# Kernel optimization log

Measured on AMD Instinct MI355X. Metric: run time of the kernel, lower is better.

## Reference

```python
import jax, jax.numpy as jnp
import numpy as np
import math

Q_SHAPES = [(20, 30), (10, 15), (5, 8)]
S_SHAPES = [(20, 30), (10, 15), (5, 8)]
C_IN = 256
C_OUT = 256
NUM_HEADS = 8


def _rel_indices(q_shapes, s_shapes):
    # Faithful translation of QSGA.get_rel_indices: block matrix over pyramid levels.
    rows = []
    for hq, wq in q_shapes:
        cols = []
        for hs, ws in s_shapes:
            ind = np.arange(ws)[None, :] / ws - np.arange(hq)[:, None] / hq  # [hq, ws]
            sc = math.sqrt(ws * hq)
            indx = np.tile(ind, (wq, hs)) * sc                              # [hq*wq, hs*ws]
            indy = np.repeat(np.repeat(ind, wq, axis=0), hs, axis=1) * sc   # [hq*wq, hs*ws]
            indd = indx ** 2 + indy ** 2
            cols.append(np.stack([indd, indx, indy], axis=-1))
        rows.append(np.concatenate(cols, axis=1))
    return jnp.asarray(np.concatenate(rows, axis=0)[None].astype(np.float32))  # [1, Nq, Ns, 3]


def setup_inputs() -> dict:
    key = jax.random.key(0)
    ks = jax.random.split(key, 8)
    B, M = 2, 5
    Nq = sum(h * w for h, w in Q_SHAPES)
    Ns = sum(h * w for h, w in S_SHAPES)
    std = 0.02
    # local_init: v = identity, pos_proj weight zero except col0 = -alphas, gating = ones
    min_a, max_a = 0.002, 0.2
    alphas = np.array([min_a + (max_a - min_a) / NUM_HEADS ** 2.5 * i ** 2.5 for i in range(NUM_HEADS)], np.float32)
    Wp = np.zeros((NUM_HEADS, 3), np.float32)
    Wp[:, 0] = -alphas
    return {
        "q_feat": jax.random.normal(ks[0], (B, Nq, C_IN), jnp.float32),
        "s_feat": jax.random.normal(ks[1], (M, Ns, C_IN), jnp.float32),
        "rel_indices": _rel_indices(Q_SHAPES, S_SHAPES),
        "Wq": jax.random.normal(ks[2], (C_OUT, C_IN), jnp.float32) * std,
        "bq": jnp.zeros((C_OUT,), jnp.float32),
        "Wk": jax.random.normal(ks[3], (C_OUT, C_IN), jnp.float32) * std,
        "bk": jnp.zeros((C_OUT,), jnp.float32),
        "Wv": jnp.eye(C_OUT, C_IN, dtype=jnp.float32),
        "bv": jnp.zeros((C_OUT,), jnp.float32),
        "Wp": jnp.asarray(Wp),
        "bp": jnp.zeros((NUM_HEADS,), jnp.float32),
        "Wo": jax.random.normal(ks[4], (C_OUT, C_OUT), jnp.float32) * std,
        "bo": jnp.zeros((C_OUT,), jnp.float32),
        "gating": jnp.ones((NUM_HEADS,), jnp.float32),
    }


def reference(q_feat, s_feat, rel_indices, Wq, bq, Wk, bk, Wv, bv, Wp, bp, Wo, bo, gating):
    B, Nq, _ = q_feat.shape
    M, Ns, _ = s_feat.shape
    H = gating.shape[0]
    C = Wq.shape[0]
    Dh = C // H
    scale = Dh ** -0.5
    # projections -> [B,H,Nq,Dh], [M,H,Ns,Dh]
    q = (q_feat @ Wq.T + bq).reshape(B, Nq, H, Dh).transpose(0, 2, 1, 3)
    k = (s_feat @ Wk.T + bk).reshape(M, Ns, H, Dh).transpose(0, 2, 1, 3)
    # content scores over all (query image, support image) pairs: [B,M,H,Nq,Ns]
    patch = jnp.einsum('bhqd,mhsd->bmhqs', q, k) * scale
    patch = jax.nn.softmax(patch, axis=-1)
    # positional scores: [1,Nq,Ns,3] -> [1,H,Nq,Ns]
    pos = jax.nn.softmax((rel_indices @ Wp.T + bp).transpose(0, 3, 1, 2), axis=-1)
    g = jax.nn.sigmoid(gating)[None, None, :, None, None]  # [1,1,H,1,1]
    attn = (1.0 - g) * patch + g * pos[:, None]            # broadcast pos over B,M
    attn = attn / attn.sum(axis=-1, keepdims=True)
    v = (s_feat @ Wv.T + bv).reshape(M, Ns, H, Dh).transpose(0, 2, 1, 3)  # [M,H,Ns,Dh]
    out = jnp.einsum('bmhqs,mhsd->bmhqd', attn, v)          # [B,M,H,Nq,Dh]
    out = out.transpose(0, 1, 3, 2, 4).reshape(B, M, Nq, C)  # [B,M,Nq,C]
    return out @ Wo.T + bo
```

## Files before the change

kernel.cpp:

```cpp
#include <hip/hip_runtime.h>
#include <hip/hip_bf16.h>
#include <math.h>

#define B_ 2
#define M_ 5
#define H_ 8
#define C_ 256
#define DH 32
#define NQ 790
#define NS 790
#define QT32 25
#define VROW 800
#define PPAD 800

typedef __attribute__((ext_vector_type(8))) __bf16 bf16x8;
typedef __attribute__((ext_vector_type(16))) float f32x16;
typedef __attribute__((ext_vector_type(2))) unsigned int u32x2;
typedef unsigned int u32;
typedef unsigned short u16;

#define LOG2E 1.4426950408889634f

static __device__ __forceinline__ u16 bf16bits(float v) {
  union { __bf16 h; u16 u; } x; x.h = (__bf16)v; return x.u;
}
static __device__ __forceinline__ u32 pack2bf(float a, float b) {
  union { __bf16 h[2]; u32 u; } x; x.h[0] = (__bf16)a; x.h[1] = (__bf16)b; return x.u;
}
static __device__ __forceinline__ float halfswap_sum(float ts) {
  union { float f; u32 u; } c; c.f = ts;
  u32x2 r = __builtin_amdgcn_permlane32_swap(c.u, c.u, false, false);
  union { u32 u; float f; } a, b; a.u = r[0]; b.u = r[1];
  return a.f + b.f;
}
static __device__ __forceinline__ void pswap(u32& x, u32& y) {
  u32x2 r = __builtin_amdgcn_permlane32_swap(x, y, false, false);
  x = r[0]; y = r[1];
}

__global__ __launch_bounds__(256) void wcvt_all(const float* __restrict__ Wq,
    const float* __restrict__ Wk, const float* __restrict__ Wv,
    const float* __restrict__ Wo,
    u16* __restrict__ wqb, u16* __restrict__ wkb, u16* __restrict__ wvb,
    u16* __restrict__ wob, u16* __restrict__ vT2) {
  int bid = blockIdx.x;
  int tid = threadIdx.x;
  if (bid == 32) {
    int c = tid;
#pragma unroll
    for (int m = 0; m < M_; ++m) {
      u32* p = (u32*)(vT2 + (size_t)c * (M_ * VROW) + m * VROW + 790);
#pragma unroll
      for (int i = 0; i < 5; ++i) p[i] = 0;
    }
    return;
  }
  int mat = bid >> 3;
  const float* src0 = (mat == 0) ? Wq : (mat == 1) ? Wk : (mat == 2) ? Wv : Wo;
  u16* dst0 = (mat == 0) ? wqb : (mat == 1) ? wkb : (mat == 2) ? wvb : wob;
  int base = (bid & 7) * 8192;
#pragma unroll
  for (int k = 0; k < 4; ++k) {
    int idx = base + k * 2048 + tid * 8;
    const float* src = src0 + idx;
    float4 f0 = *(const float4*)src, f1 = *(const float4*)(src + 4);
    u16 v[8];
    v[0]=bf16bits(f0.x); v[1]=bf16bits(f0.y); v[2]=bf16bits(f0.z); v[3]=bf16bits(f0.w);
    v[4]=bf16bits(f1.x); v[5]=bf16bits(f1.y); v[6]=bf16bits(f1.z); v[7]=bf16bits(f1.w);
    *(uint4*)(dst0 + idx) = *(uint4*)v;
  }
}

#define GEMM_N 149
#define POS0 149

#define PROJ_STEP(ACC, BY)                                                 \
  {                                                                        \
    int bcol_ = (BY) * 64 + wc * 32 + lo;                                  \
    bf16x8 b_ = *(const bf16x8*)(Wmb + (size_t)bcol_ * C_ + k0);           \
    ACC = __builtin_amdgcn_mfma_f32_32x32x16_bf16(a_, b_, ACC, 0, 0, 0);   \
  }

#define STORE_QK(ACC, BY)                                                  \
  {                                                                        \
    int bcol_ = (BY) * 64 + wc * 32 + lo;                                  \
    float bvv_ = bias[bcol_];                                              \
    _Pragma("unroll")                                                      \
    for (int r_ = 0; r_ < 16; ++r_) {                                      \
      int row_ = (r_ & 3) + 8 * (r_ >> 2) + 4 * hi;                        \
      int grow_ = grow0 + wr * 32 + row_;                                  \
      if (grow_ < R) {                                                     \
        float v_ = (ACC[r_] + bvv_) * scale;                               \
        int seg_ = grow_ / 790, srow_ = grow_ - seg_ * 790;                \
        size_t addr_ = ((size_t)(seg_ * H_ + (bcol_ >> 5)) * 790 + srow_) * 32 + (bcol_ & 31); \
        outp[addr_] = bf16bits(v_);                                        \
      }                                                                    \
    }                                                                      \
  }

#define STORE_V(ACC, BY)                                                   \
  {                                                                        \
    int bcol_ = (BY) * 64 + wc * 32 + lo;                                  \
    float bvv_ = bias[bcol_];                                              \
    int cIn_ = wc * 32 + lo;                                               \
    _Pragma("unroll")                                                      \
    for (int r_ = 0; r_ < 16; ++r_) {                                      \
      int row_ = (r_ & 3) + 8 * (r_ >> 2) + 4 * hi;                        \
      Tls[cIn_][wr * 32 + row_] = bf16bits(ACC[r_] + bvv_);                \
    }                                                                      \
    __syncthreads();                                                       \
    {                                                                      \
      int c_l = tid >> 2, g_l = (tid & 3) * 16;                            \
      int gcol = (BY) * 64 + c_l;                                          \
      int g0v = grow0 + g_l;                                               \
      u16 vals_[16];                                                       \
      _Pragma("unroll")                                                    \
      for (int i_ = 0; i_ < 16; ++i_) vals_[i_] = Tls[c_l][g_l + i_];      \
      int mA_ = g0v / 790, mB_ = (g0v + 15) / 790;                         \
      u16* dst_ = vT2 + (size_t)gcol * (M_ * VROW);                        \
      if (mB_ < M_ && mA_ == mB_) {                                        \
        size_t base_ = (size_t)mA_ * VROW + (g0v - mA_ * 790);             \
        *(uint4*)(dst_ + base_)     = *(uint4*)(vals_);                    \
        *(uint4*)(dst_ + base_ + 8) = *(uint4*)(vals_ + 8);                \
      } else {                                                             \
        _Pragma("unroll")                                                  \
        for (int i_ = 0; i_ < 16; ++i_) {                                  \
          int g_ = g0v + i_;                                               \
          if (g_ < M_ * 790) {                                             \
            int mm_ = g_ / 790, ss_ = g_ - mm_ * 790;                      \
            dst_[(size_t)mm_ * VROW + ss_] = vals_[i_];                    \
          }                                                                \
        }                                                                  \
      }                                                                    \
    }                                                                      \
    __syncthreads();                                                       \
  }

__global__ __launch_bounds__(256) void stage1(const float* __restrict__ qf,
    const float* __restrict__ sf, const float* __restrict__ rel,
    const u16* __restrict__ wqb, const float* __restrict__ bq,
    const u16* __restrict__ wkb, const float* __restrict__ bk,
    const u16* __restrict__ wvb, const float* __restrict__ bv,
    const float* __restrict__ Wp, const float* __restrict__ bp,
    u16* __restrict__ qb, u16* __restrict__ kb, u16* __restrict__ vT2,
    u16* __restrict__ pp, float qscale) {
  __shared__ u16 Tls[64][72];
  int bid = blockIdx.x;
  int tid = threadIdx.x;

  if (bid < GEMM_N) {
    int j = bid;
    const float* A; const u16* Wmb; const float* bias; int R; float scale; int role; int bx;
    if (j < 25)      { A = qf; Wmb = wqb; bias = bq; R = B_ * NQ; scale = qscale; role = 0; bx = j; }
    else if (j < 87) { A = sf; Wmb = wkb; bias = bk; R = M_ * NS; scale = 1.f;    role = 1; bx = j - 25; }
    else             { A = sf; Wmb = wvb; bias = bv; R = M_ * NS; scale = 1.f;    role = 2; bx = j - 87; }

    int wave = tid >> 6, lane = tid & 63;
    int lo = lane & 31, hi = lane >> 5;
    int wr = wave >> 1, wc = wave & 1;
    int grow0 = bx * 64;
    int arow = grow0 + wr * 32 + lo;
    int ar = arow < R ? arow : R - 1;

    f32x16 acc0, acc1, acc2, acc3;
#pragma unroll
    for (int r = 0; r < 16; ++r) { acc0[r] = 0.f; acc1[r] = 0.f; acc2[r] = 0.f; acc3[r] = 0.f; }
#pragma unroll
    for (int kk = 0; kk < 16; ++kk) {
      int k0 = kk * 16 + hi * 8;
      const float* af = A + (size_t)ar * C_ + k0;
      float4 f0 = *(const float4*)af, f1 = *(const float4*)(af + 4);
      bf16x8 a_;
      a_[0]=(__bf16)f0.x; a_[1]=(__bf16)f0.y; a_[2]=(__bf16)f0.z; a_[3]=(__bf16)f0.w;
      a_[4]=(__bf16)f1.x; a_[5]=(__bf16)f1.y; a_[6]=(__bf16)f1.z; a_[7]=(__bf16)f1.w;
      PROJ_STEP(acc0, 0);
      PROJ_STEP(acc1, 1);
      PROJ_STEP(acc2, 2);
      PROJ_STEP(acc3, 3);
    }

    if (role < 2) {
      u16* outp = (role == 0) ? qb : kb;
      STORE_QK(acc0, 0);
      STORE_QK(acc1, 1);
      STORE_QK(acc2, 2);
      STORE_QK(acc3, 3);
    } else {
      STORE_V(acc0, 0);
      STORE_V(acc1, 1);
      STORE_V(acc2, 2);
      STORE_V(acc3, 3);
    }
    return;
  }

  {
    int pj = bid - POS0;
    int wave = tid >> 6, lane = tid & 63;
    int q = pj * 2 + (wave >> 1);
    int h0 = (wave & 1) * 4;
    float rd[13], rx[13], ry[13];
#pragma unroll
    for (int t = 0; t < 13; ++t) {
      int s = lane + 64 * t;
      if (s < NS) {
        const float* rp = rel + ((size_t)q * NS + s) * 3;
        rd[t] = rp[0]; rx[t] = rp[1]; ry[t] = rp[2];
      } else { rd[t] = 0.f; rx[t] = 0.f; ry[t] = 0.f; }
    }
    for (int h = h0; h < h0 + 4; ++h) {
      float w0 = Wp[h * 3] * LOG2E, w1 = Wp[h * 3 + 1] * LOG2E,
            w2 = Wp[h * 3 + 2] * LOG2E, b = bp[h] * LOG2E;
      float lg[13], sm = 0.f;
#pragma unroll
      for (int t = 0; t < 13; ++t) {
        int s = lane + 64 * t;
        float v = rd[t] * w0 + rx[t] * w1 + ry[t] * w2 + b;
        lg[t] = exp2f((s < NS) ? v : -1e30f);
        sm += lg[t];
      }
#pragma unroll
      for (int off = 32; off; off >>= 1) sm += __shfl_xor(sm, off);
      float inv = 1.f / sm;
#pragma unroll
      for (int t = 0; t < 13; ++t) {
        int s = lane + 64 * t;
        if (s < PPAD)
          pp[((size_t)h * NQ + q) * PPAD + s] = (s < NS) ? bf16bits(lg[t] * inv) : (u16)0;
      }
    }
  }
}

static __device__ __forceinline__ void wave_range(int wave, int& st, int& en) {
  st = wave * 6 + (wave ? 1 : 0);
  en = st + (wave ? 6 : 7);
}

#define SM_PV(c_, OACC, ZR, FV0, FV1)                                      \
  {                                                                        \
    float p_[16];                                                          \
    _Pragma("unroll")                                                      \
    for (int r_ = 0; r_ < 16; ++r_) p_[r_] = exp2f(c_[r_]);                \
    float s0_ = p_[0]+p_[1],  s1_ = p_[2]+p_[3];                           \
    float s2_ = p_[4]+p_[5],  s3_ = p_[6]+p_[7];                           \
    float s4_ = p_[8]+p_[9],  s5_ = p_[10]+p_[11];                         \
    float s6_ = p_[12]+p_[13], s7_ = p_[14]+p_[15];                        \
    s0_ += s1_; s2_ += s3_; s4_ += s5_; s6_ += s7_;                        \
    s0_ += s2_; s4_ += s6_;                                                \
    ZR += halfswap_sum(s0_ + s4_);                                         \
    u32 pk_[8];                                                            \
    _Pragma("unroll")                                                      \
    for (int t_ = 0; t_ < 8; ++t_) pk_[t_] = pack2bf(p_[2*t_], p_[2*t_+1]); \
    pswap(pk_[0], pk_[2]);                                                 \
    pswap(pk_[1], pk_[3]);                                                 \
    pswap(pk_[4], pk_[6]);                                                 \
    pswap(pk_[5], pk_[7]);                                                 \
    union { u32 u[4]; bf16x8 v; } pa_, pb_;                                \
    pa_.u[0] = pk_[0]; pa_.u[1] = pk_[1]; pa_.u[2] = pk_[2]; pa_.u[3] = pk_[3]; \
    pb_.u[0] = pk_[4]; pb_.u[1] = pk_[5]; pb_.u[2] = pk_[6]; pb_.u[3] = pk_[7]; \
    OACC = __builtin_amdgcn_mfma_f32_32x32x16_bf16(FV0, pa_.v, OACC, 0, 0, 0); \
    OACC = __builtin_amdgcn_mfma_f32_32x32x16_bf16(FV1, pb_.v, OACC, 0, 0, 0); \
  }

#define TILE_BODY(KC0,KC1, KN0,KN1, IT, NT)                                \
  {                                                                        \
    bf16x8 vf0 = *(const bf16x8*)(vbase + (IT) * 32 + hi8);                \
    bf16x8 vf1 = *(const bf16x8*)(vbase + (IT) * 32 + 16 + hi8);           \
    bf16x8 pf0 = *(const bf16x8*)(pbase + (IT) * 32 + hi8);                \
    bf16x8 pf1 = *(const bf16x8*)(pbase + (IT) * 32 + 16 + hi8);           \
    int srn_ = (NT) * 32 + lo; if (srn_ >= NS) srn_ = NS - 1;              \
    KN0 = *(const bf16x8*)(kbase + (size_t)srn_ * 32 + hi8);               \
    KN1 = *(const bf16x8*)(kbase + (size_t)srn_ * 32 + 16 + hi8);          \
    f32x16 c0_, c1_;                                                       \
    _Pragma("unroll")                                                      \
    for (int r_ = 0; r_ < 16; ++r_) { c0_[r_] = 0.f; c1_[r_] = 0.f; }      \
    c0_ = __builtin_amdgcn_mfma_f32_32x32x16_bf16(KC0, fq00, c0_, 0, 0, 0);\
    c0_ = __builtin_amdgcn_mfma_f32_32x32x16_bf16(KC1, fq01, c0_, 0, 0, 0);\
    c1_ = __builtin_amdgcn_mfma_f32_32x32x16_bf16(KC0, fq10, c1_, 0, 0, 0);\
    c1_ = __builtin_amdgcn_mfma_f32_32x32x16_bf16(KC1, fq11, c1_, 0, 0, 0);\
    if ((IT) == 24) {                                                      \
      _Pragma("unroll")                                                    \
      for (int r_ = 0; r_ < 16; ++r_) {                                    \
        int sl_ = (r_ & 3) + 8 * (r_ >> 2) + 4 * hi;                       \
        if (768 + sl_ >= NS) { c0_[r_] = -1e30f; c1_[r_] = -1e30f; }       \
      }                                                                    \
    }                                                                      \
    SM_PV(c0_, O0, Z0, vf0, vf1);                                          \
    Opos = __builtin_amdgcn_mfma_f32_32x32x16_bf16(vf0, pf0, Opos, 0, 0, 0);\
    Opos = __builtin_amdgcn_mfma_f32_32x32x16_bf16(vf1, pf1, Opos, 0, 0, 0);\
    SM_PV(c1_, O1, Z1, vf0, vf1);                                          \
  }

__global__ __launch_bounds__(256, 3) void attn2(const u16* __restrict__ qb,
    const u16* __restrict__ kb, const u16* __restrict__ vT2,
    const u16* __restrict__ pp, const float* __restrict__ gating,
    u16* __restrict__ opb) {
  int logical = (blockIdx.x & 7) * 125 + (blockIdx.x >> 3);
  int m  = logical % M_;
  int r2 = logical / M_;
  int qt = r2 % QT32;
  int h  = r2 / QT32;
  int tid = threadIdx.x;
  int wave = tid >> 6, lane = tid & 63;
  int lo = lane & 31, hi = lane >> 5, hi8 = hi * 8;
  int qg = qt * 32 + lo;
  int qc = qg < NQ ? qg : NQ - 1;

  const u16* qp0 = qb + ((size_t)(0 * H_ + h) * NQ + qc) * 32 + hi8;
  const u16* qp1 = qb + ((size_t)(1 * H_ + h) * NQ + qc) * 32 + hi8;
  bf16x8 fq00 = *(const bf16x8*)qp0;
  bf16x8 fq01 = *(const bf16x8*)(qp0 + 16);
  bf16x8 fq10 = *(const bf16x8*)qp1;
  bf16x8 fq11 = *(const bf16x8*)(qp1 + 16);
  const u16* kbase = kb + ((size_t)(m * H_ + h) * NS) * 32;
  const u16* vbase = vT2 + (size_t)(h * DH + lo) * (M_ * VROW) + m * VROW;
  const u16* pbase = pp + ((size_t)h * NQ + qc) * PPAD;

  f32x16 O0, O1, Opos;
#pragma unroll
  for (int r = 0; r < 16; ++r) { O0[r] = 0.f; O1[r] = 0.f; Opos[r] = 0.f; }
  float Z0 = 0.f, Z1 = 0.f;
  int st, en; wave_range(wave, st, en);

  bf16x8 ak0, ak1, bk0, bk1;
  {
    int sr0 = st * 32 + lo; if (sr0 >= NS) sr0 = NS - 1;
    ak0 = *(const bf16x8*)(kbase + (size_t)sr0 * 32 + hi8);
    ak1 = *(const bf16x8*)(kbase + (size_t)sr0 * 32 + 16 + hi8);
  }
  int it = st;
  while (it + 2 <= en) {
    TILE_BODY(ak0, ak1, bk0, bk1, it, it + 1);
    int nt2 = (it + 2 < en) ? it + 2 : it + 1;
    TILE_BODY(bk0, bk1, ak0, ak1, it + 1, nt2);
    it += 2;
  }
  if (it < en) TILE_BODY(ak0, ak1, bk0, bk1, it, it);

  __shared__ float Os[4][32][33];
  __shared__ float Zs[4][32];
  float g = 1.f / (1.f + __expf(-gating[h]));
  int d = tid & 31, qi = tid >> 5;
  float oc0[4], oc1[4];

#pragma unroll
  for (int r = 0; r < 16; ++r) {
    int dd = (r & 3) + 8 * (r >> 2) + 4 * hi;
    Os[wave][dd][lo] = O0[r];
  }
  if (hi == 0) Zs[wave][lo] = Z0;
  __syncthreads();
#pragma unroll
  for (int k = 0; k < 4; ++k) {
    int ql = qi + 8 * k;
    float zg = Zs[0][ql] + Zs[1][ql] + Zs[2][ql] + Zs[3][ql];
    float oc = Os[0][d][ql] + Os[1][d][ql] + Os[2][d][ql] + Os[3][d][ql];
    oc0[k] = (1.f - g) * oc / zg;
  }
  __syncthreads();

#pragma unroll
  for (int r = 0; r < 16; ++r) {
    int dd = (r & 3) + 8 * (r >> 2) + 4 * hi;
    Os[wave][dd][lo] = O1[r];
  }
  if (hi == 0) Zs[wave][lo] = Z1;
  __syncthreads();
#pragma unroll
  for (int k = 0; k < 4; ++k) {
    int ql = qi + 8 * k;
    float zg = Zs[0][ql] + Zs[1][ql] + Zs[2][ql] + Zs[3][ql];
    float oc = Os[0][d][ql] + Os[1][d][ql] + Os[2][d][ql] + Os[3][d][ql];
    oc1[k] = (1.f - g) * oc / zg;
  }
  __syncthreads();

#pragma unroll
  for (int r = 0; r < 16; ++r) {
    int dd = (r & 3) + 8 * (r >> 2) + 4 * hi;
    Os[wave][dd][lo] = Opos[r];
  }
  __syncthreads();
  u16* out0 = opb + ((size_t)(0 * M_ + m) * NQ) * C_ + h * DH + d;
  u16* out1 = opb + ((size_t)(1 * M_ + m) * NQ) * C_ + h * DH + d;
#pragma unroll
  for (int k = 0; k < 4; ++k) {
    int ql = qi + 8 * k;
    int qgl = qt * 32 + ql;
    if (qgl < NQ) {
      float op = Os[0][d][ql] + Os[1][d][ql] + Os[2][d][ql] + Os[3][d][ql];
      out0[(size_t)qgl * C_] = bf16bits(oc0[k] + g * op);
      out1[(size_t)qgl * C_] = bf16bits(oc1[k] + g * op);
    }
  }
}

__global__ __launch_bounds__(256) void out_gemm(const u16* __restrict__ Ap,
    const u16* __restrict__ Wb, const float* __restrict__ bias,
    float* __restrict__ outp, int R) {
  int tid = threadIdx.x;
  int wave = tid >> 6, lane = tid & 63;
  int lo = lane & 31, hi = lane >> 5;
  int wr = wave >> 1, wc = wave & 1;
  int arow = blockIdx.x * 64 + wr * 32 + lo;
  int ar = arow < R ? arow : R - 1;
  int bcolA = blockIdx.y * 128 + wc * 32 + lo;
  int bcolB = bcolA + 64;
  f32x16 accA, accB;
#pragma unroll
  for (int r = 0; r < 16; ++r) { accA[r] = 0.f; accB[r] = 0.f; }
#pragma unroll
  for (int kk = 0; kk < 16; ++kk) {
    int k0 = kk * 16 + hi * 8;
    bf16x8 a = *(const bf16x8*)(Ap + (size_t)ar * C_ + k0);
    bf16x8 bA = *(const bf16x8*)(Wb + (size_t)bcolA * C_ + k0);
    bf16x8 bB = *(const bf16x8*)(Wb + (size_t)bcolB * C_ + k0);
    accA = __builtin_amdgcn_mfma_f32_32x32x16_bf16(a, bA, accA, 0, 0, 0);
    accB = __builtin_amdgcn_mfma_f32_32x32x16_bf16(a, bB, accB, 0, 0, 0);
  }
  float bvA = bias[bcolA], bvB = bias[bcolB];
#pragma unroll
  for (int r = 0; r < 16; ++r) {
    int row = (r & 3) + 8 * (r >> 2) + 4 * hi;
    int grow = blockIdx.x * 64 + wr * 32 + row;
    if (grow < R) {
      outp[(size_t)grow * C_ + bcolA] = accA[r] + bvA;
      outp[(size_t)grow * C_ + bcolB] = accB[r] + bvB;
    }
  }
}

extern "C" void kernel_launch(void* const* d_in, const int* in_sizes, int n_in,
                              void* d_out, int out_size, void* d_ws, size_t ws_size,
                              hipStream_t stream) {
  const float* q_feat = (const float*)d_in[0];
  const float* s_feat = (const float*)d_in[1];
  const float* rel    = (const float*)d_in[2];
  const float* Wq = (const float*)d_in[3];
  const float* bq = (const float*)d_in[4];
  const float* Wk = (const float*)d_in[5];
  const float* bk = (const float*)d_in[6];
  const float* Wv = (const float*)d_in[7];
  const float* bv = (const float*)d_in[8];
  const float* Wp = (const float*)d_in[9];
  const float* bp = (const float*)d_in[10];
  const float* Wo = (const float*)d_in[11];
  const float* bo = (const float*)d_in[12];
  const float* gating = (const float*)d_in[13];
  float* out = (float*)d_out;

  char* w = (char*)d_ws;
  u16* qb  = (u16*)w;
  u16* kb  = (u16*)(w + 808960);
  u16* vT2 = (u16*)(w + 2831360);
  u16* pp  = (u16*)(w + 4879360);
  u16* opb = (u16*)(w + 14991360);
  u16* wob = (u16*)(w + 19036160);
  u16* wqb = (u16*)(w + 19167232);
  u16* wkb = (u16*)(w + 19298304);
  u16* wvb = (u16*)(w + 19429376);

  const float QSCALE = 0.17677669529663687f * 1.4426950408889634f;

  wcvt_all<<<33, 256, 0, stream>>>(Wq, Wk, Wv, Wo, wqb, wkb, wvb, wob, vT2);
  stage1<<<544, 256, 0, stream>>>(q_feat, s_feat, rel, wqb, bq, wkb, bk, wvb, bv,
                                  Wp, bp, qb, kb, vT2, pp, QSCALE);
  attn2<<<1000, 256, 0, stream>>>(qb, kb, vT2, pp, gating, opb);
  out_gemm<<<dim3(124, 2), 256, 0, stream>>>(opb, wob, bo, out, B_ * M_ * NQ);
}
```

Measured before the change: 68.51 us.

## Vectorize positional softmax stores, add MFMA priority hints, merge epilogue barriers

The positional-softmax branch now handles two adjacent support positions per lane and writes them as one packed 32-bit bf16 store instead of scalar 16-bit stores. In the attention kernel, s_setprio raises wave priority around MFMA groups to encourage overlap with other waves' softmax work. The epilogue stages O0, O1 and Opos into a larger shared buffer with a single barrier instead of five, at the cost of about three times more LDS per block. That extra LDS could limit occupancy under the 3-blocks-per-CU launch bound.

Result: no change. 68.59 us (+0.1%).

```diff
diff --git a/kernel.cpp b/kernel.cpp
--- a/kernel.cpp
+++ b/kernel.cpp
@@ -199,34 +199,43 @@
     int wave = tid >> 6, lane = tid & 63;
     int q = pj * 2 + (wave >> 1);
     int h0 = (wave & 1) * 4;
-    float rd[13], rx[13], ry[13];
-#pragma unroll
-    for (int t = 0; t < 13; ++t) {
-      int s = lane + 64 * t;
-      if (s < NS) {
-        const float* rp = rel + ((size_t)q * NS + s) * 3;
-        rd[t] = rp[0]; rx[t] = rp[1]; ry[t] = rp[2];
-      } else { rd[t] = 0.f; rx[t] = 0.f; ry[t] = 0.f; }
+    float rd0[7], rx0[7], ry0[7], rd1[7], rx1[7], ry1[7];
+#pragma unroll
+    for (int t = 0; t < 7; ++t) {
+      int s0 = 2 * lane + 128 * t;
+      int s1 = s0 + 1;
+      if (s0 < NS) {
+        const float* rp = rel + ((size_t)q * NS + s0) * 3;
+        rd0[t] = rp[0]; rx0[t] = rp[1]; ry0[t] = rp[2];
+        if (s1 < NS) { rd1[t] = rp[3]; rx1[t] = rp[4]; ry1[t] = rp[5]; }
+        else         { rd1[t] = 0.f; rx1[t] = 0.f; ry1[t] = 0.f; }
+      } else {
+        rd0[t] = 0.f; rx0[t] = 0.f; ry0[t] = 0.f;
+        rd1[t] = 0.f; rx1[t] = 0.f; ry1[t] = 0.f;
+      }
     }
     for (int h = h0; h < h0 + 4; ++h) {
       float w0 = Wp[h * 3] * LOG2E, w1 = Wp[h * 3 + 1] * LOG2E,
             w2 = Wp[h * 3 + 2] * LOG2E, b = bp[h] * LOG2E;
-      float lg[13], sm = 0.f;
-#pragma unroll
-      for (int t = 0; t < 13; ++t) {
-        int s = lane + 64 * t;
-        float v = rd[t] * w0 + rx[t] * w1 + ry[t] * w2 + b;
-        lg[t] = exp2f((s < NS) ? v : -1e30f);
-        sm += lg[t];
+      float e0[7], e1[7], sm = 0.f;
+#pragma unroll
+      for (int t = 0; t < 7; ++t) {
+        int s0 = 2 * lane + 128 * t;
+        float v0 = rd0[t] * w0 + rx0[t] * w1 + ry0[t] * w2 + b;
+        float v1 = rd1[t] * w0 + rx1[t] * w1 + ry1[t] * w2 + b;
+        e0[t] = (s0 < NS)     ? exp2f(v0) : 0.f;
+        e1[t] = (s0 + 1 < NS) ? exp2f(v1) : 0.f;
+        sm += e0[t] + e1[t];
       }
 #pragma unroll
       for (int off = 32; off; off >>= 1) sm += __shfl_xor(sm, off);
       float inv = 1.f / sm;
-#pragma unroll
-      for (int t = 0; t < 13; ++t) {
-        int s = lane + 64 * t;
-        if (s < PPAD)
-          pp[((size_t)h * NQ + q) * PPAD + s] = (s < NS) ? bf16bits(lg[t] * inv) : (u16)0;
+      u16* row = pp + ((size_t)h * NQ + q) * PPAD;
+#pragma unroll
+      for (int t = 0; t < 7; ++t) {
+        int s0 = 2 * lane + 128 * t;
+        if (s0 < PPAD)
+          *(u32*)(row + s0) = pack2bf(e0[t] * inv, e1[t] * inv);
       }
     }
   }
@@ -259,8 +268,10 @@
     union { u32 u[4]; bf16x8 v; } pa_, pb_;                                \
     pa_.u[0] = pk_[0]; pa_.u[1] = pk_[1]; pa_.u[2] = pk_[2]; pa_.u[3] = pk_[3]; \
     pb_.u[0] = pk_[4]; pb_.u[1] = pk_[5]; pb_.u[2] = pk_[6]; pb_.u[3] = pk_[7]; \
+    __builtin_amdgcn_s_setprio(1);                                         \
     OACC = __builtin_amdgcn_mfma_f32_32x32x16_bf16(FV0, pa_.v, OACC, 0, 0, 0); \
     OACC = __builtin_amdgcn_mfma_f32_32x32x16_bf16(FV1, pb_.v, OACC, 0, 0, 0); \
+    __builtin_amdgcn_s_setprio(0);                                         \
   }
 
 #define TILE_BODY(KC0,KC1, KN0,KN1, IT, NT)                                \
@@ -275,10 +286,12 @@
     f32x16 c0_, c1_;                                                       \
     _Pragma("unroll")                                                      \
     for (int r_ = 0; r_ < 16; ++r_) { c0_[r_] = 0.f; c1_[r_] = 0.f; }      \
+    __builtin_amdgcn_s_setprio(1);                                         \
     c0_ = __builtin_amdgcn_mfma_f32_32x32x16_bf16(KC0, fq00, c0_, 0, 0, 0);\
     c0_ = __builtin_amdgcn_mfma_f32_32x32x16_bf16(KC1, fq01, c0_, 0, 0, 0);\
     c1_ = __builtin_amdgcn_mfma_f32_32x32x16_bf16(KC0, fq10, c1_, 0, 0, 0);\
     c1_ = __builtin_amdgcn_mfma_f32_32x32x16_bf16(KC1, fq11, c1_, 0, 0, 0);\
+    __builtin_amdgcn_s_setprio(0);                                         \
     if ((IT) == 24) {                                                      \
       _Pragma("unroll")                                                    \
       for (int r_ = 0; r_ < 16; ++r_) {                                    \
@@ -287,8 +300,10 @@
       }                                                                    \
     }                                                                      \
     SM_PV(c0_, O0, Z0, vf0, vf1);                                          \
+    __builtin_amdgcn_s_setprio(1);                                         \
     Opos = __builtin_amdgcn_mfma_f32_32x32x16_bf16(vf0, pf0, Opos, 0, 0, 0);\
     Opos = __builtin_amdgcn_mfma_f32_32x32x16_bf16(vf1, pf1, Opos, 0, 0, 0);\
+    __builtin_amdgcn_s_setprio(0);                                         \
     SM_PV(c1_, O1, Z1, vf0, vf1);                                          \
   }
 
@@ -338,50 +353,20 @@
   }
   if (it < en) TILE_BODY(ak0, ak1, bk0, bk1, it, it);
 
-  __shared__ float Os[4][32][33];
-  __shared__ float Zs[4][32];
+  __shared__ float Os[3][4][32][33];
+  __shared__ float Zs[2][4][32];
+#pragma unroll
+  for (int r = 0; r < 16; ++r) {
+    int dd = (r & 3) + 8 * (r >> 2) + 4 * hi;
+    Os[0][wave][dd][lo] = O0[r];
+    Os[1][wave][dd][lo] = O1[r];
+    Os[2][wave][dd][lo] = Opos[r];
+  }
+  if (hi == 0) { Zs[0][wave][lo] = Z0; Zs[1][wave][lo] = Z1; }
+  __syncthreads();
+
   float g = 1.f / (1.f + __expf(-gating[h]));
   int d = tid & 31, qi = tid >> 5;
-  float oc0[4], oc1[4];
-
-#pragma unroll
-  for (int r = 0; r < 16; ++r) {
-    int dd = (r & 3) + 8 * (r >> 2) + 4 * hi;
-    Os[wave][dd][lo] = O0[r];
-  }
-  if (hi == 0) Zs[wave][lo] = Z0;
-  __syncthreads();
-#pragma unroll
-  for (int k = 0; k < 4; ++k) {
-    int ql = qi + 8 * k;
-    float zg = Zs[0][ql] + Zs[1][ql] + Zs[2][ql] + Zs[3][ql];
-    float oc = Os[0][d][ql] + Os[1][d][ql] + Os[2][d][ql] + Os[3][d][ql];
-    oc0[k] = (1.f - g) * oc / zg;
-  }
-  __syncthreads();
-
-#pragma unroll
-  for (int r = 0; r < 16; ++r) {
-    int dd = (r & 3) + 8 * (r >> 2) + 4 * hi;
-    Os[wave][dd][lo] = O1[r];
-  }
-  if (hi == 0) Zs[wave][lo] = Z1;
-  __syncthreads();
-#pragma unroll
-  for (int k = 0; k < 4; ++k) {
-    int ql = qi + 8 * k;
-    float zg = Zs[0][ql] + Zs[1][ql] + Zs[2][ql] + Zs[3][ql];
-    float oc = Os[0][d][ql] + Os[1][d][ql] + Os[2][d][ql] + Os[3][d][ql];
-    oc1[k] = (1.f - g) * oc / zg;
-  }
-  __syncthreads();
-
-#pragma unroll
-  for (int r = 0; r < 16; ++r) {
-    int dd = (r & 3) + 8 * (r >> 2) + 4 * hi;
-    Os[wave][dd][lo] = Opos[r];
-  }
-  __syncthreads();
   u16* out0 = opb + ((size_t)(0 * M_ + m) * NQ) * C_ + h * DH + d;
   u16* out1 = opb + ((size_t)(1 * M_ + m) * NQ) * C_ + h * DH + d;
 #pragma unroll
@@ -389,9 +374,13 @@
     int ql = qi + 8 * k;
     int qgl = qt * 32 + ql;
     if (qgl < NQ) {
-      float op = Os[0][d][ql] + Os[1][d][ql] + Os[2][d][ql] + Os[3][d][ql];
-      out0[(size_t)qgl * C_] = bf16bits(oc0[k] + g * op);
-      out1[(size_t)qgl * C_] = bf16bits(oc1[k] + g * op);
+      float zg0 = Zs[0][0][ql] + Zs[0][1][ql] + Zs[0][2][ql] + Zs[0][3][ql];
+      float zg1 = Zs[1][0][ql] + Zs[1][1][ql] + Zs[1][2][ql] + Zs[1][3][ql];
+      float oc0 = Os[0][0][d][ql] + Os[0][1][d][ql] + Os[0][2][d][ql] + Os[0][3][d][ql];
+      float oc1 = Os[1][0][d][ql] + Os[1][1][d][ql] + Os[1][2][d][ql] + Os[1][3][d][ql];
+      float op  = Os[2][0][d][ql] + Os[2][1][d][ql] + Os[2][2][d][ql] + Os[2][3][d][ql];
+      out0[(size_t)qgl * C_] = bf16bits((1.f - g) * oc0 / zg0 + g * op);
+      out1[(size_t)qgl * C_] = bf16bits((1.f - g) * oc1 / zg1 + g * op);
     }
   }
 }
```
